# Kernel tuning notes

Hardware: AMD Instinct MI355X
Metric: run time of the kernel (lower is better)

The kernel has to match this reference:

```python
import jax, jax.numpy as jnp
import numpy as np

S, B, D, H, FF, L, V, O = 512, 32, 512, 8, 2048, 6, 32000, 1000
DH = D // H
EPS = 1e-5


def layer_norm(x, g, b):
    mu = jnp.mean(x, axis=-1, keepdims=True)
    var = jnp.mean((x - mu) ** 2, axis=-1, keepdims=True)
    return (x - mu) * jax.lax.rsqrt(var + EPS) * g + b


def positional_encoding(seq_len, dim):
    pos = np.arange(seq_len, dtype=np.float32)[:, None]
    i = np.arange(dim)
    angle = pos / (10000.0 ** ((i // 2 * 2.0) / dim))
    pe = np.where(i % 2 == 0, np.sin(angle), np.cos(angle)).astype(np.float32)
    return jnp.asarray(pe)  # [seq_len, dim]


def setup_inputs() -> dict:
    key = jax.random.key(0)
    ks = jax.random.split(key, 16)
    sc = 0.02
    inp = {
        'x': jax.random.randint(ks[0], (S, B), 0, V, dtype=jnp.int32),
        'x_len': jnp.full((B,), S, dtype=jnp.int32),
        'emb': jax.random.normal(ks[1], (V, D), jnp.float32) * sc,
        'Wq': jax.random.normal(ks[2], (L, D, D), jnp.float32) * sc,
        'bq': jnp.zeros((L, D), jnp.float32),
        'Wk': jax.random.normal(ks[3], (L, D, D), jnp.float32) * sc,
        'bk': jnp.zeros((L, D), jnp.float32),
        'Wv': jax.random.normal(ks[4], (L, D, D), jnp.float32) * sc,
        'bv': jnp.zeros((L, D), jnp.float32),
        'Wo': jax.random.normal(ks[5], (L, D, D), jnp.float32) * sc,
        'bo': jnp.zeros((L, D), jnp.float32),
        'ln1_g': jnp.ones((L, D), jnp.float32),
        'ln1_b': jnp.zeros((L, D), jnp.float32),
        'W1': jax.random.normal(ks[6], (L, D, FF), jnp.float32) * sc,
        'b1': jnp.zeros((L, FF), jnp.float32),
        'W2': jax.random.normal(ks[7], (L, FF, D), jnp.float32) * sc,
        'b2': jnp.zeros((L, D), jnp.float32),
        'ln2_g': jnp.ones((L, D), jnp.float32),
        'ln2_b': jnp.zeros((L, D), jnp.float32),
        'W_fc': jax.random.normal(ks[8], (S * D, O), jnp.float32) * sc,
        'b_fc': jnp.zeros((O,), jnp.float32),
    }
    return inp


def reference(x, x_len, emb, Wq, bq, Wk, bk, Wv, bv, Wo, bo, ln1_g, ln1_b,
              W1, b1, W2, b2, ln2_g, ln2_b, W_fc, b_fc):
    out = emb[x]                      # [S, B, D]
    out = jnp.transpose(out, (1, 0, 2))  # [B, S, D]
    out = out + positional_encoding(S, D)[None, :, :]
    scale = DH ** -0.5
    for l in range(L):
        # NOTE: faithful to the original buggy head-split: plain row-major
        # reshape [B,S,D] -> [B*H,S,DH] without a [B,H,S,DH] transpose.
        q = jnp.reshape(out @ Wq[l] + bq[l], (B * H, S, DH))
        k = jnp.reshape(out @ Wk[l] + bk[l], (B * H, S, DH))
        v = jnp.reshape(out @ Wv[l] + bv[l], (B * H, S, DH))
        attn = jax.nn.softmax(jnp.einsum('gqd,gkd->gqk', q, k) * scale, axis=-1)
        ctx = jnp.einsum('gqk,gkd->gqd', attn, v).reshape(B, S, D)
        h = layer_norm(ctx @ Wo[l] + bo[l] + out, ln1_g[l], ln1_b[l])
        f = jax.nn.relu(h @ W1[l] + b1[l]) @ W2[l] + b2[l]
        out = layer_norm(f + h, ln2_g[l], ln2_b[l])
    out = out.reshape(B, S * D)
    return out @ W_fc + b_fc          # [B, O]
```

## Files before the change

### kernel.cpp

```cpp
#include <hip/hip_runtime.h>
#include <cstdint>
#include <cstddef>

#define S_  512
#define B_  32
#define D_  512
#define FF_ 2048
#define L_  6
#define O_  1000
#define M_  (B_*S_)
#define G_  256
#define DH_ 64

typedef __attribute__((ext_vector_type(8))) short bf16x8;
typedef __attribute__((ext_vector_type(4))) float f32x4;
typedef __attribute__((ext_vector_type(16))) float f32x16;

__device__ __forceinline__ unsigned short f2bf(float f) {
  unsigned int u = __builtin_bit_cast(unsigned int, f);
  u = (u + 0x7fffu + ((u >> 16) & 1u)) >> 16;
  return (unsigned short)u;
}
__device__ __forceinline__ float bf2f(unsigned short u) {
  return __builtin_bit_cast(float, (unsigned int)u << 16);
}
__device__ __forceinline__ unsigned int pkbf(float a, float b) {
  return (unsigned int)f2bf(a) | ((unsigned int)f2bf(b) << 16);
}
__device__ __forceinline__ void gload_lds16(const void* g, void* l) {
  __builtin_amdgcn_global_load_lds(
      (const __attribute__((address_space(1))) unsigned int*)g,
      (__attribute__((address_space(3))) unsigned int*)l, 16, 0, 0);
}

__global__ void pe_kernel(float* __restrict__ pe) {
  int i = blockIdx.x * 256 + threadIdx.x;
  int s = i >> 9, d = i & 511;
  double de = (double)(d & ~1);
  double ang = (double)s * exp(de * (-9.210340371976184 / 512.0));
  pe[i] = (d & 1) ? (float)cos(ang) : (float)sin(ang);
}

__global__ void wconv_kernel(const float* __restrict__ W, unsigned short* __restrict__ Wt,
                             int K, int N, size_t ozs) {
  __shared__ float tile[32][33];
  const float* Wl = W + (size_t)blockIdx.z * K * N;
  unsigned short* Wtl = Wt + (size_t)blockIdx.z * ozs;
  int k0 = blockIdx.x * 32, n0 = blockIdx.y * 32;
  int c = threadIdx.x & 31, rb = threadIdx.x >> 5;
#pragma unroll
  for (int i = 0; i < 4; ++i) {
    int r = rb + i * 8;
    tile[r][c] = Wl[(size_t)(k0 + r) * N + n0 + c];
  }
  __syncthreads();
#pragma unroll
  for (int i = 0; i < 4; ++i) {
    int r = rb + i * 8;
    Wtl[(size_t)(n0 + r) * K + k0 + c] = f2bf(tile[c][r]);
  }
}

__global__ void embed_kernel(const int* __restrict__ x, const float* __restrict__ emb,
                             const float* __restrict__ pe, unsigned short* __restrict__ xb) {
  int bi = blockIdx.x;
  int s = bi / B_, b = bi % B_;
  int tok = x[s * B_ + b];
  int d = threadIdx.x * 4;
  float4 e = *(const float4*)(emb + (size_t)tok * D_ + d);
  float4 p = *(const float4*)(pe + (size_t)s * D_ + d);
  size_t o = ((size_t)b * S_ + s) * D_ + d;
  ushort4 u;
  u.x = f2bf(e.x + p.x); u.y = f2bf(e.y + p.y);
  u.z = f2bf(e.z + p.z); u.w = f2bf(e.w + p.w);
  *(ushort4*)(xb + o) = u;
}

__global__ __launch_bounds__(256, 2) void gemm_kernel(
    const unsigned short* __restrict__ A, const unsigned short* __restrict__ Bt,
    const float* __restrict__ b0, const float* __restrict__ b1, const float* __restrict__ b2,
    unsigned short* __restrict__ o0, unsigned short* __restrict__ o1, unsigned short* __restrict__ o2,
    int K, int N, int relu, int split, int nbx) {
  __shared__ unsigned short As[3][128 * 32];
  __shared__ unsigned short Bs[3][256 * 32];
  int nwg = nbx * (M_ / 128);
  int cpx = nwg >> 3;
  int id = blockIdx.x;
  int wg = (id & 7) * cpx + (id >> 3);
  int bx = wg % nbx, by = wg / nbx;
  int m0 = by * 128, n0 = bx * 256;

  int tid = threadIdx.x, lane = tid & 63, wid = tid >> 6;
  f32x4 acc[8][4];
#pragma unroll
  for (int mi = 0; mi < 8; ++mi)
#pragma unroll
    for (int ni = 0; ni < 4; ++ni) acc[mi][ni] = (f32x4)0.0f;

  int srow = lane >> 2, scol = (lane & 3) * 8;
  const unsigned short* Abase = A + (size_t)m0 * K;
  const unsigned short* Bbase = Bt + (size_t)n0 * K;
  int c16 = lane & 15, hi = lane >> 4;
  int koff = hi * 8;
  int brow = wid * 64 + c16;
  int nk = K >> 5;

  auto STAGE = [&](int kt, int bb) {
    int k0 = kt * 32;
#pragma unroll
    for (int i = 0; i < 6; ++i) {
      int c = wid * 6 + i;
      if (c < 8) {
        gload_lds16(Abase + (size_t)(c * 16 + srow) * K + k0 + scol, (char*)As[bb] + c * 1024);
      } else {
        int c2 = c - 8;
        gload_lds16(Bbase + (size_t)(c2 * 16 + srow) * K + k0 + scol, (char*)Bs[bb] + c2 * 1024);
      }
    }
  };

  STAGE(0, 0); STAGE(1, 1); STAGE(2, 2);
  int bb = 0;
  for (int kt = 0; kt < nk; ++kt) {
    int rem = nk - 1 - kt;
    if (rem >= 2)      asm volatile("s_waitcnt vmcnt(12)" ::: "memory");
    else if (rem == 1) asm volatile("s_waitcnt vmcnt(6)" ::: "memory");
    else               asm volatile("s_waitcnt vmcnt(0)" ::: "memory");
    __builtin_amdgcn_s_barrier();
    __builtin_amdgcn_sched_barrier(0);
    bf16x8 af[8], bfr[4];
#pragma unroll
    for (int mi = 0; mi < 8; ++mi) af[mi] = *(const bf16x8*)&As[bb][(mi * 16 + c16) * 32 + koff];
#pragma unroll
    for (int ni = 0; ni < 4; ++ni) bfr[ni] = *(const bf16x8*)&Bs[bb][(brow + ni * 16) * 32 + koff];
    __builtin_amdgcn_s_setprio(1);
#pragma unroll
    for (int mi = 0; mi < 8; ++mi)
#pragma unroll
      for (int ni = 0; ni < 4; ++ni)
        acc[mi][ni] = __builtin_amdgcn_mfma_f32_16x16x32_bf16(bfr[ni], af[mi], acc[mi][ni], 0, 0, 0);
    __builtin_amdgcn_s_setprio(0);
    __builtin_amdgcn_sched_barrier(0);
    __builtin_amdgcn_s_barrier();
    if (kt + 3 < nk) STAGE(kt + 3, bb);
    bb = (bb == 2) ? 0 : bb + 1;
  }

  const float* bias = b0;
  unsigned short* outb = o0;
  int nbase = n0, ostride = N;
  if (split) {
    int seg = n0 >> 9;
    if (seg == 1) { bias = b1; outb = o1; }
    else if (seg == 2) { bias = b2; outb = o2; }
    nbase = n0 & 511; ostride = 512;
  }
#pragma unroll
  for (int ni = 0; ni < 4; ++ni) {
    int colb = nbase + wid * 64 + ni * 16 + hi * 4;
    float4 bv = *(const float4*)(bias + colb);
#pragma unroll
    for (int mi = 0; mi < 8; ++mi) {
      int row = m0 + mi * 16 + c16;
      float v0 = acc[mi][ni][0] + bv.x;
      float v1 = acc[mi][ni][1] + bv.y;
      float v2 = acc[mi][ni][2] + bv.z;
      float v3 = acc[mi][ni][3] + bv.w;
      if (relu) { v0 = fmaxf(v0, 0.f); v1 = fmaxf(v1, 0.f); v2 = fmaxf(v2, 0.f); v3 = fmaxf(v3, 0.f); }
      *(uint2*)(outb + (size_t)row * ostride + colb) = make_uint2(pkbf(v0, v1), pkbf(v2, v3));
    }
  }
}

__global__ __launch_bounds__(128) void addln_kernel(
    const unsigned short* __restrict__ Y, const unsigned short* __restrict__ R,
    const float* __restrict__ g, const float* __restrict__ b,
    unsigned short* __restrict__ Out) {
  __shared__ float red[2], red2[2];
  int row = blockIdx.x, t = threadIdx.x;
  size_t o = (size_t)row * 512 + t * 4;
  ushort4 yv = *(const ushort4*)(Y + o);
  ushort4 rv = *(const ushort4*)(R + o);
  float v0 = bf2f(yv.x) + bf2f(rv.x);
  float v1 = bf2f(yv.y) + bf2f(rv.y);
  float v2 = bf2f(yv.z) + bf2f(rv.z);
  float v3 = bf2f(yv.w) + bf2f(rv.w);
  float s = v0 + v1 + v2 + v3;
#pragma unroll
  for (int m = 1; m < 64; m <<= 1) s += __shfl_xor(s, m);
  if ((t & 63) == 0) red[t >> 6] = s;
  __syncthreads();
  float mean = (red[0] + red[1]) * (1.0f / 512.0f);
  float d0 = v0 - mean, d1 = v1 - mean, d2 = v2 - mean, d3 = v3 - mean;
  float sq = d0 * d0 + d1 * d1 + d2 * d2 + d3 * d3;
#pragma unroll
  for (int m = 1; m < 64; m <<= 1) sq += __shfl_xor(sq, m);
  if ((t & 63) == 0) red2[t >> 6] = sq;
  __syncthreads();
  float var = (red2[0] + red2[1]) * (1.0f / 512.0f);
  float rstd = rsqrtf(var + 1e-5f);
  float4 gg = *(const float4*)(g + t * 4);
  float4 bb = *(const float4*)(b + t * 4);
  float y0 = d0 * rstd * gg.x + bb.x;
  float y1 = d1 * rstd * gg.y + bb.y;
  float y2 = d2 * rstd * gg.z + bb.z;
  float y3 = d3 * rstd * gg.w + bb.w;
  *(uint2*)(Out + o) = make_uint2(pkbf(y0, y1), pkbf(y2, y3));
}

__global__ __launch_bounds__(256) void attn_kernel(
    const unsigned short* __restrict__ Q, const unsigned short* __restrict__ Kb,
    const unsigned short* __restrict__ Vb, unsigned short* __restrict__ Ctx) {
  __shared__ char KlB[8192];
  __shared__ char VtB[8192];
  int g = blockIdx.y;
  int q0 = blockIdx.x * 256;
  const unsigned short* Kg = Kb + (size_t)g * 512 * 64;
  const unsigned short* Vg = Vb + (size_t)g * 512 * 64;
  int tid = threadIdx.x, lane = tid & 63, wid = tid >> 6;
  int l31 = lane & 31, h = lane >> 5;
  bool lo = (lane < 32);
  int qrowA = q0 + wid * 64 + l31;
  int qrowB = qrowA + 32;
  const float sc2 = 0.125f * 1.44269504f;

  bf16x8 qfa[4], qfb[4];
  {
    const unsigned short* qpa = Q + ((size_t)g * 512 + qrowA) * 64;
    const unsigned short* qpb = Q + ((size_t)g * 512 + qrowB) * 64;
#pragma unroll
    for (int c = 0; c < 4; ++c) {
      bf16x8 ra = *(const bf16x8*)(qpa + c * 16 + h * 8);
      bf16x8 rb = *(const bf16x8*)(qpb + c * 16 + h * 8);
      union { unsigned int u[4]; bf16x8 v; } ua, ub;
#pragma unroll
      for (int j = 0; j < 4; ++j) {
        ua.u[j] = pkbf(bf2f((unsigned short)ra[2 * j]) * sc2,
                       bf2f((unsigned short)ra[2 * j + 1]) * sc2);
        ub.u[j] = pkbf(bf2f((unsigned short)rb[2 * j]) * sc2,
                       bf2f((unsigned short)rb[2 * j + 1]) * sc2);
      }
      qfa[c] = ua.v; qfb[c] = ub.v;
    }
  }

  f32x16 cA0 = (f32x16)0.0f, cA1 = (f32x16)0.0f;
  f32x16 cB0 = (f32x16)0.0f, cB1 = (f32x16)0.0f;
  float mrA = -3.0e38f, lsA = 0.0f;
  float mrB = -3.0e38f, lsB = 0.0f;

  for (int kt = 0; kt < 8; ++kt) {
    __syncthreads();
    {
      int row = tid >> 2;
      size_t base = (size_t)(kt * 64 + row) * 64;
#pragma unroll
      for (int i = 0; i < 2; ++i) {
        int cb = ((tid & 3) + 4 * i) * 16;
        bf16x8 kv = *(const bf16x8*)(Kg + base + cb / 2);
        *(bf16x8*)(KlB + row * 128 + (cb ^ ((row & 7) << 4))) = kv;
        bf16x8 vv = *(const bf16x8*)(Vg + base + cb / 2);
#pragma unroll
        for (int j = 0; j < 8; ++j) {
          int d = cb / 2 + j;
          *(unsigned short*)(VtB + d * 128 + ((2 * row) ^ ((d & 7) << 4))) =
              (unsigned short)vv[j];
        }
      }
    }
    __syncthreads();

#pragma unroll
    for (int sub = 0; sub < 2; ++sub) {
      f32x16 s0 = (f32x16)0.0f, s1 = (f32x16)0.0f;
#pragma unroll
      for (int c = 0; c < 4; ++c) {
        int cb = 32 * c + 16 * h;
        int sw = cb ^ ((l31 & 7) << 4);
        bf16x8 k0 = *(const bf16x8*)(KlB + l31 * 128 + sw);
        bf16x8 k1 = *(const bf16x8*)(KlB + (32 + l31) * 128 + sw);
        bf16x8 qf = sub ? qfb[c] : qfa[c];
        s0 = __builtin_amdgcn_mfma_f32_32x32x16_bf16(k0, qf, s0, 0, 0, 0);
        s1 = __builtin_amdgcn_mfma_f32_32x32x16_bf16(k1, qf, s1, 0, 0, 0);
      }

      float mr = sub ? mrB : mrA;
      float ls = sub ? lsB : lsA;
      float pm = s0[0];
#pragma unroll
      for (int i = 1; i < 16; ++i) pm = fmaxf(pm, s0[i]);
#pragma unroll
      for (int i = 0; i < 16; ++i) pm = fmaxf(pm, s1[i]);
      pm = fmaxf(pm, __shfl_xor(pm, 32));
      float mnew = fmaxf(mr, pm);
      float alpha = exp2f(mr - mnew);
      float p[32];
      float rs = 0.0f;
#pragma unroll
      for (int i = 0; i < 16; ++i) { p[i] = exp2f(s0[i] - mnew); rs += p[i]; }
#pragma unroll
      for (int i = 0; i < 16; ++i) { p[16 + i] = exp2f(s1[i] - mnew); rs += p[16 + i]; }
      float rso = __shfl_xor(rs, 32);
      ls = ls * alpha + rs + rso;
      if (sub) { mrB = mnew; lsB = ls; } else { mrA = mnew; lsA = ls; }
      if (sub) {
#pragma unroll
        for (int i = 0; i < 16; ++i) { cB0[i] *= alpha; cB1[i] *= alpha; }
      } else {
#pragma unroll
        for (int i = 0; i < 16; ++i) { cA0[i] *= alpha; cA1[i] *= alpha; }
      }

      union { unsigned int u[4]; bf16x8 v; } pa[4];
#pragma unroll
      for (int t = 0; t < 2; ++t) {
#pragma unroll
        for (int u = 0; u < 2; ++u) {
#pragma unroll
          for (int pr = 0; pr < 2; ++pr) {
            const int b0i = t * 16 + 8 * u;
            unsigned int a  = pkbf(p[b0i + 2 * pr],     p[b0i + 2 * pr + 1]);
            unsigned int b  = pkbf(p[b0i + 4 + 2 * pr], p[b0i + 4 + 2 * pr + 1]);
            unsigned int sa = __shfl_xor(a, 32);
            unsigned int sb = __shfl_xor(b, 32);
            pa[t * 2 + u].u[pr]     = lo ? a  : sb;
            pa[t * 2 + u].u[2 + pr] = lo ? sa : b;
          }
        }
      }

#pragma unroll
      for (int kc = 0; kc < 4; ++kc) {
        int cb = 32 * kc + 16 * h;
        int sw = cb ^ ((l31 & 7) << 4);
        bf16x8 v0 = *(const bf16x8*)(VtB + l31 * 128 + sw);
        bf16x8 v1 = *(const bf16x8*)(VtB + (32 + l31) * 128 + sw);
        if (sub) {
          cB0 = __builtin_amdgcn_mfma_f32_32x32x16_bf16(v0, pa[kc].v, cB0, 0, 0, 0);
          cB1 = __builtin_amdgcn_mfma_f32_32x32x16_bf16(v1, pa[kc].v, cB1, 0, 0, 0);
        } else {
          cA0 = __builtin_amdgcn_mfma_f32_32x32x16_bf16(v0, pa[kc].v, cA0, 0, 0, 0);
          cA1 = __builtin_amdgcn_mfma_f32_32x32x16_bf16(v1, pa[kc].v, cA1, 0, 0, 0);
        }
      }
    }
  }

#pragma unroll
  for (int sub = 0; sub < 2; ++sub) {
    float inv = 1.0f / (sub ? lsB : lsA);
    int qrow = sub ? qrowB : qrowA;
    unsigned short* cp = Ctx + ((size_t)g * 512 + qrow) * 64;
#pragma unroll
    for (int dh = 0; dh < 2; ++dh) {
#pragma unroll
      for (int rq = 0; rq < 4; ++rq) {
        float e0 = (sub ? (dh ? cB1[rq * 4 + 0] : cB0[rq * 4 + 0]) : (dh ? cA1[rq * 4 + 0] : cA0[rq * 4 + 0])) * inv;
        float e1 = (sub ? (dh ? cB1[rq * 4 + 1] : cB0[rq * 4 + 1]) : (dh ? cA1[rq * 4 + 1] : cA0[rq * 4 + 1])) * inv;
        float e2 = (sub ? (dh ? cB1[rq * 4 + 2] : cB0[rq * 4 + 2]) : (dh ? cA1[rq * 4 + 2] : cA0[rq * 4 + 2])) * inv;
        float e3 = (sub ? (dh ? cB1[rq * 4 + 3] : cB0[rq * 4 + 3]) : (dh ? cA1[rq * 4 + 3] : cA0[rq * 4 + 3])) * inv;
        int d0 = dh * 32 + rq * 8 + h * 4;
        *(uint2*)(cp + d0) = make_uint2(pkbf(e0, e1), pkbf(e2, e3));
      }
    }
  }
}

#define KCH 1024
__global__ __launch_bounds__(256) void fc_part_kernel(const unsigned short* __restrict__ act,
                                                      const float* __restrict__ Wfc,
                                                      float* __restrict__ part) {
  __shared__ float al[32][256];
  int o = blockIdx.x * 256 + threadIdx.x;
  int kc = blockIdx.y;
  size_t k0 = (size_t)kc * KCH;
  float acc[32];
#pragma unroll
  for (int bb = 0; bb < 32; ++bb) acc[bb] = 0.0f;
  for (int sub = 0; sub < KCH / 256; ++sub) {
    __syncthreads();
    for (int i = threadIdx.x; i < 32 * 128; i += 256) {
      int bb = i >> 7, kk = (i & 127) * 2;
      ushort2 u = *(const ushort2*)(act + (size_t)bb * 262144 + k0 + sub * 256 + kk);
      al[bb][kk] = bf2f(u.x);
      al[bb][kk + 1] = bf2f(u.y);
    }
    __syncthreads();
    if (o < O_) {
      const float* wp = Wfc + (k0 + sub * 256) * O_ + o;
      for (int kk = 0; kk < 256; ++kk) {
        float w = wp[(size_t)kk * O_];
#pragma unroll
        for (int bb = 0; bb < 32; ++bb) acc[bb] = fmaf(al[bb][kk], w, acc[bb]);
      }
    }
  }
  if (o < O_) {
#pragma unroll
    for (int bb = 0; bb < 32; ++bb) part[((size_t)kc * 32 + bb) * O_ + o] = acc[bb];
  }
}

__global__ void fc_reduce_kernel(const float* __restrict__ part, const float* __restrict__ bfc,
                                 float* __restrict__ out) {
  int o = blockIdx.x * 256 + threadIdx.x;
  int b = blockIdx.y;
  if (o >= O_) return;
  float s = bfc[o];
  for (int c = 0; c < 256; ++c) s += part[((size_t)c * 32 + b) * O_ + o];
  out[(size_t)b * O_ + o] = s;
}

extern "C" void kernel_launch(void* const* d_in, const int* in_sizes, int n_in,
                              void* d_out, int out_size, void* d_ws, size_t ws_size,
                              hipStream_t stream) {
  const int*   x   = (const int*)d_in[0];
  const float* emb = (const float*)d_in[2];
  const float* Wq  = (const float*)d_in[3];
  const float* bq  = (const float*)d_in[4];
  const float* Wk  = (const float*)d_in[5];
  const float* bk  = (const float*)d_in[6];
  const float* Wv  = (const float*)d_in[7];
  const float* bv  = (const float*)d_in[8];
  const float* Wo  = (const float*)d_in[9];
  const float* bo  = (const float*)d_in[10];
  const float* g1  = (const float*)d_in[11];
  const float* bn1 = (const float*)d_in[12];
  const float* W1  = (const float*)d_in[13];
  const float* bf1 = (const float*)d_in[14];
  const float* W2  = (const float*)d_in[15];
  const float* bf2 = (const float*)d_in[16];
  const float* g2  = (const float*)d_in[17];
  const float* bn2 = (const float*)d_in[18];
  const float* Wfc = (const float*)d_in[19];
  const float* bfc = (const float*)d_in[20];
  float* out = (float*)d_out;

  char* ws = (char*)d_ws;
  size_t off = 0;
  auto take = [&](size_t bytes) { char* p = ws + off; off += (bytes + 255) & ~(size_t)255; return p; };
  float*          pe   = (float*)take((size_t)512 * 512 * 4);
  unsigned short* wqkv = (unsigned short*)take((size_t)L_ * 1536 * 512 * 2);
  unsigned short* wot  = (unsigned short*)take((size_t)L_ * 512 * 512 * 2);
  unsigned short* w1t  = (unsigned short*)take((size_t)L_ * 2048 * 512 * 2);
  unsigned short* w2t  = (unsigned short*)take((size_t)L_ * 512 * 2048 * 2);
  unsigned short* xb   = (unsigned short*)take((size_t)M_ * 512 * 2);
  unsigned short* qb   = (unsigned short*)take((size_t)M_ * 512 * 2);
  unsigned short* kb   = (unsigned short*)take((size_t)M_ * 512 * 2);
  unsigned short* vb   = (unsigned short*)take((size_t)M_ * 512 * 2);
  unsigned short* cxb  = (unsigned short*)take((size_t)M_ * 512 * 2);
  unsigned short* hb   = (unsigned short*)take((size_t)M_ * 512 * 2);
  unsigned short* t1   = (unsigned short*)take((size_t)M_ * 512 * 2);
  unsigned short* f1b  = qb;
  float*          part = (float*)qb;

  pe_kernel<<<1024, 256, 0, stream>>>(pe);
  wconv_kernel<<<dim3(16, 16, L_), 256, 0, stream>>>(Wq, wqkv,          512, 512,  (size_t)1536 * 512);
  wconv_kernel<<<dim3(16, 16, L_), 256, 0, stream>>>(Wk, wqkv + 262144, 512, 512,  (size_t)1536 * 512);
  wconv_kernel<<<dim3(16, 16, L_), 256, 0, stream>>>(Wv, wqkv + 524288, 512, 512,  (size_t)1536 * 512);
  wconv_kernel<<<dim3(16, 16, L_), 256, 0, stream>>>(Wo, wot,           512, 512,  (size_t)512 * 512);
  wconv_kernel<<<dim3(16, 64, L_), 256, 0, stream>>>(W1, w1t,           512, 2048, (size_t)2048 * 512);
  wconv_kernel<<<dim3(64, 16, L_), 256, 0, stream>>>(W2, w2t,           2048, 512, (size_t)512 * 2048);
  embed_kernel<<<M_, 128, 0, stream>>>(x, emb, pe, xb);

  for (int l = 0; l < L_; ++l) {
    gemm_kernel<<<768, 256, 0, stream>>>(
        xb, wqkv + (size_t)l * 1536 * 512,
        bq + l * 512, bk + l * 512, bv + l * 512,
        qb, kb, vb, 512, 1536, 0, 1, 6);
    attn_kernel<<<dim3(2, G_), 256, 0, stream>>>(qb, kb, vb, cxb);
    gemm_kernel<<<256, 256, 0, stream>>>(
        cxb, wot + (size_t)l * 512 * 512,
        bo + l * 512, nullptr, nullptr,
        t1, nullptr, nullptr, 512, 512, 0, 0, 2);
    addln_kernel<<<M_, 128, 0, stream>>>(t1, xb, g1 + l * 512, bn1 + l * 512, hb);
    gemm_kernel<<<1024, 256, 0, stream>>>(
        hb, w1t + (size_t)l * 2048 * 512,
        bf1 + l * 2048, nullptr, nullptr,
        f1b, nullptr, nullptr, 512, 2048, 1, 0, 8);
    gemm_kernel<<<256, 256, 0, stream>>>(
        f1b, w2t + (size_t)l * 512 * 2048,
        bf2 + l * 512, nullptr, nullptr,
        t1, nullptr, nullptr, 2048, 512, 0, 0, 2);
    addln_kernel<<<M_, 128, 0, stream>>>(t1, hb, g2 + l * 512, bn2 + l * 512, xb);
  }

  fc_part_kernel<<<dim3(4, 256), 256, 0, stream>>>(xb, Wfc, part);
  fc_reduce_kernel<<<dim3(4, 32), 256, 0, stream>>>(part, bfc, out);
}
```

Before: 2.121 ms.

## Lazy softmax rescale, truncating bf16 pack, and restructured FC partial kernel

In attention, the running max and the rescaling of the accumulators are now updated only when some lane's new block max exceeds the stored max by more than 8 (log2 units), so most tiles skip the alpha multiply. Packing P to bf16 now uses a byte-permute truncation instead of round-to-nearest, which makes the pack cheaper but adds a small rounding bias. The FC partial kernel now runs 512 threads per block, each thread covering two output columns and four k rows per step with vectorised LDS reads, so every LDS load of activations is reused across more FMAs and fewer blocks are launched. Occupancy may drop because of register pressure from 64 accumulators per thread.

```diff
diff --git a/kernel.cpp b/kernel.cpp
--- a/kernel.cpp
+++ b/kernel.cpp
@@ -26,6 +26,10 @@
 }
 __device__ __forceinline__ unsigned int pkbf(float a, float b) {
   return (unsigned int)f2bf(a) | ((unsigned int)f2bf(b) << 16);
+}
+__device__ __forceinline__ unsigned int prm(float a, float b) {
+  return __builtin_amdgcn_perm(__builtin_bit_cast(unsigned int, b),
+                               __builtin_bit_cast(unsigned int, a), 0x07060302u);
 }
 __device__ __forceinline__ void gload_lds16(const void* g, void* l) {
   __builtin_amdgcn_global_load_lds(
@@ -292,24 +296,28 @@
 #pragma unroll
       for (int i = 0; i < 16; ++i) pm = fmaxf(pm, s1[i]);
       pm = fmaxf(pm, __shfl_xor(pm, 32));
-      float mnew = fmaxf(mr, pm);
-      float alpha = exp2f(mr - mnew);
+      if (!__all(pm <= mr + 8.0f)) {
+        float mnew = fmaxf(mr, pm);
+        float alpha = exp2f(mr - mnew);
+        ls *= alpha;
+        if (sub) {
+#pragma unroll
+          for (int i = 0; i < 16; ++i) { cB0[i] *= alpha; cB1[i] *= alpha; }
+        } else {
+#pragma unroll
+          for (int i = 0; i < 16; ++i) { cA0[i] *= alpha; cA1[i] *= alpha; }
+        }
+        mr = mnew;
+      }
       float p[32];
       float rs = 0.0f;
 #pragma unroll
-      for (int i = 0; i < 16; ++i) { p[i] = exp2f(s0[i] - mnew); rs += p[i]; }
-#pragma unroll
-      for (int i = 0; i < 16; ++i) { p[16 + i] = exp2f(s1[i] - mnew); rs += p[16 + i]; }
+      for (int i = 0; i < 16; ++i) { p[i] = exp2f(s0[i] - mr); rs += p[i]; }
+#pragma unroll
+      for (int i = 0; i < 16; ++i) { p[16 + i] = exp2f(s1[i] - mr); rs += p[16 + i]; }
       float rso = __shfl_xor(rs, 32);
-      ls = ls * alpha + rs + rso;
-      if (sub) { mrB = mnew; lsB = ls; } else { mrA = mnew; lsA = ls; }
-      if (sub) {
-#pragma unroll
-        for (int i = 0; i < 16; ++i) { cB0[i] *= alpha; cB1[i] *= alpha; }
-      } else {
-#pragma unroll
-        for (int i = 0; i < 16; ++i) { cA0[i] *= alpha; cA1[i] *= alpha; }
-      }
+      ls += rs + rso;
+      if (sub) { mrB = mr; lsB = ls; } else { mrA = mr; lsA = ls; }
 
       union { unsigned int u[4]; bf16x8 v; } pa[4];
 #pragma unroll
@@ -319,8 +327,8 @@
 #pragma unroll
           for (int pr = 0; pr < 2; ++pr) {
             const int b0i = t * 16 + 8 * u;
-            unsigned int a  = pkbf(p[b0i + 2 * pr],     p[b0i + 2 * pr + 1]);
-            unsigned int b  = pkbf(p[b0i + 4 + 2 * pr], p[b0i + 4 + 2 * pr + 1]);
+            unsigned int a  = prm(p[b0i + 2 * pr],     p[b0i + 2 * pr + 1]);
+            unsigned int b  = prm(p[b0i + 4 + 2 * pr], p[b0i + 4 + 2 * pr + 1]);
             unsigned int sa = __shfl_xor(a, 32);
             unsigned int sb = __shfl_xor(b, 32);
             pa[t * 2 + u].u[pr]     = lo ? a  : sb;
@@ -367,37 +375,57 @@
 }
 
 #define KCH 1024
-__global__ __launch_bounds__(256) void fc_part_kernel(const unsigned short* __restrict__ act,
+__global__ __launch_bounds__(512) void fc_part_kernel(const unsigned short* __restrict__ act,
                                                       const float* __restrict__ Wfc,
                                                       float* __restrict__ part) {
   __shared__ float al[32][256];
-  int o = blockIdx.x * 256 + threadIdx.x;
-  int kc = blockIdx.y;
+  int t = threadIdx.x;
+  int kc = blockIdx.x;
   size_t k0 = (size_t)kc * KCH;
-  float acc[32];
-#pragma unroll
-  for (int bb = 0; bb < 32; ++bb) acc[bb] = 0.0f;
+  int o1 = t;
+  int o2 = 512 + t;
+  bool a2 = (o2 < O_);
+  float acc1[32], acc2[32];
+#pragma unroll
+  for (int bb = 0; bb < 32; ++bb) { acc1[bb] = 0.0f; acc2[bb] = 0.0f; }
   for (int sub = 0; sub < KCH / 256; ++sub) {
     __syncthreads();
-    for (int i = threadIdx.x; i < 32 * 128; i += 256) {
+    for (int i = t; i < 32 * 128; i += 512) {
       int bb = i >> 7, kk = (i & 127) * 2;
       ushort2 u = *(const ushort2*)(act + (size_t)bb * 262144 + k0 + sub * 256 + kk);
       al[bb][kk] = bf2f(u.x);
       al[bb][kk + 1] = bf2f(u.y);
     }
     __syncthreads();
-    if (o < O_) {
-      const float* wp = Wfc + (k0 + sub * 256) * O_ + o;
-      for (int kk = 0; kk < 256; ++kk) {
-        float w = wp[(size_t)kk * O_];
-#pragma unroll
-        for (int bb = 0; bb < 32; ++bb) acc[bb] = fmaf(al[bb][kk], w, acc[bb]);
-      }
-    }
-  }
-  if (o < O_) {
-#pragma unroll
-    for (int bb = 0; bb < 32; ++bb) part[((size_t)kc * 32 + bb) * O_ + o] = acc[bb];
+    const float* wp = Wfc + (k0 + sub * 256) * O_;
+    for (int kk = 0; kk < 256; kk += 4) {
+      const float* wr = wp + (size_t)kk * O_;
+      float w10 = wr[o1];
+      float w11 = wr[O_ + o1];
+      float w12 = wr[2 * O_ + o1];
+      float w13 = wr[3 * O_ + o1];
+      float w20 = a2 ? wr[o2] : 0.0f;
+      float w21 = a2 ? wr[O_ + o2] : 0.0f;
+      float w22 = a2 ? wr[2 * O_ + o2] : 0.0f;
+      float w23 = a2 ? wr[3 * O_ + o2] : 0.0f;
+#pragma unroll
+      for (int bb = 0; bb < 32; ++bb) {
+        f32x4 av = *(const f32x4*)&al[bb][kk];
+        acc1[bb] = fmaf(av[0], w10, acc1[bb]);
+        acc1[bb] = fmaf(av[1], w11, acc1[bb]);
+        acc1[bb] = fmaf(av[2], w12, acc1[bb]);
+        acc1[bb] = fmaf(av[3], w13, acc1[bb]);
+        acc2[bb] = fmaf(av[0], w20, acc2[bb]);
+        acc2[bb] = fmaf(av[1], w21, acc2[bb]);
+        acc2[bb] = fmaf(av[2], w22, acc2[bb]);
+        acc2[bb] = fmaf(av[3], w23, acc2[bb]);
+      }
+    }
+  }
+#pragma unroll
+  for (int bb = 0; bb < 32; ++bb) {
+    part[((size_t)kc * 32 + bb) * O_ + o1] = acc1[bb];
+    if (a2) part[((size_t)kc * 32 + bb) * O_ + o2] = acc2[bb];
   }
 }
 
@@ -485,6 +513,6 @@
     addln_kernel<<<M_, 128, 0, stream>>>(t1, hb, g2 + l * 512, bn2 + l * 512, xb);
   }
 
-  fc_part_kernel<<<dim3(4, 256), 256, 0, stream>>>(xb, Wfc, part);
+  fc_part_kernel<<<256, 512, 0, stream>>>(xb, Wfc, part);
   fc_reduce_kernel<<<dim3(4, 32), 256, 0, stream>>>(part, bfc, out);
 }
```

Measured after the change: 1.942 ms. -8.4%, faster.
